# Kernel tuning notes

Hardware: AMD Instinct MI355X
Metric: run time of the kernel (lower is better)

## Reference

```python
import jax, jax.numpy as jnp
import numpy as np

OBS, ACT, HID, P, B = 128, 32, 256, 64, 4096
EPS = 1e-5


def _block(x, W, b, g, be, act=True):
    # x: [B, P, Din]; W: [P, Din, Dout]; b/g/be: [P, Dout]
    y = jnp.einsum('bpi,pio->bpo', x, W) + b
    # GroupNorm with one group per sub-policy: normalize over Dout per (b, p)
    mu = jnp.mean(y, axis=-1, keepdims=True)
    var = jnp.var(y, axis=-1, keepdims=True)
    y = (y - mu) * jax.lax.rsqrt(var + EPS) * g + be
    return jax.nn.elu(y) if act else y


def setup_inputs() -> dict:
    key = jax.random.key(0)
    ks = jax.random.split(key, 17)
    s = 0.05
    return {
        'observation': jax.random.normal(ks[0], (B, OBS), dtype=jnp.float32),
        'W1': jax.random.normal(ks[1], (P, OBS, HID), dtype=jnp.float32) * s,
        'b1': jax.random.normal(ks[2], (P, HID), dtype=jnp.float32) * s,
        'g1': jnp.ones((P, HID), dtype=jnp.float32),
        'be1': jnp.zeros((P, HID), dtype=jnp.float32),
        'W2': jax.random.normal(ks[3], (P, HID, HID), dtype=jnp.float32) * s,
        'b2': jax.random.normal(ks[4], (P, HID), dtype=jnp.float32) * s,
        'g2': jnp.ones((P, HID), dtype=jnp.float32),
        'be2': jnp.zeros((P, HID), dtype=jnp.float32),
        'W3': jax.random.normal(ks[5], (P, HID, HID), dtype=jnp.float32) * s,
        'b3': jax.random.normal(ks[6], (P, HID), dtype=jnp.float32) * s,
        'g3': jnp.ones((P, HID), dtype=jnp.float32),
        'be3': jnp.zeros((P, HID), dtype=jnp.float32),
        'W4': jax.random.normal(ks[7], (P, HID, ACT), dtype=jnp.float32) * s,
        'b4': jax.random.normal(ks[8], (P, ACT), dtype=jnp.float32) * s,
        'g4': jnp.ones((P, ACT), dtype=jnp.float32),
        'be4': jnp.zeros((P, ACT), dtype=jnp.float32),
    }


def reference(observation, W1, b1, g1, be1, W2, b2, g2, be2,
              W3, b3, g3, be3, W4, b4, g4, be4):
    # broadcast observation to each sub-policy: [B, P, OBS]
    x = jnp.broadcast_to(observation[:, None, :], (observation.shape[0], P, OBS))
    x = _block(x, W1, b1, g1, be1, act=True)
    x = _block(x, W2, b2, g2, be2, act=True)
    x = _block(x, W3, b3, g3, be3, act=True)
    x = _block(x, W4, b4, g4, be4, act=False)
    return x  # [B, P, ACT] action logits
```

## Files before the change

### kernel.cpp

```cpp
#include <hip/hip_runtime.h>

#define B_    4096
#define P_    64
#define OBS_  128
#define HID_  256
#define ACTD_ 32

typedef __attribute__((ext_vector_type(8)))  __bf16 bf16x8;
typedef __attribute__((ext_vector_type(2)))  __bf16 bf16x2_t;
typedef __attribute__((ext_vector_type(2)))  float  f32x2;
typedef __attribute__((ext_vector_type(4)))  float  f32x4;
typedef __attribute__((ext_vector_type(16))) float  f32x16;

#define XSTRIDE 264

#define WS1 0L
#define WS2 2097152L
#define WS3 6291456L
#define WS4 10485760L

#if defined(__has_builtin)
#if __has_builtin(__builtin_amdgcn_cvt_pk_bf16_f32)
#define HAVE_CVT_PK_BF16 1
#endif
#endif
#ifndef HAVE_CVT_PK_BF16
#define HAVE_CVT_PK_BF16 0
#endif

__device__ __forceinline__ unsigned short f2bf(float x) {
    unsigned u = __builtin_bit_cast(unsigned, x);
    u = (u + 0x7fffu + ((u >> 16) & 1u)) >> 16;
    return (unsigned short)u;
}

__device__ __forceinline__ unsigned pack_bf16_rne(float a, float b) {
#if HAVE_CVT_PK_BF16
    bf16x2_t p = __builtin_amdgcn_cvt_pk_bf16_f32(a, b);
    return __builtin_bit_cast(unsigned, p);
#else
    unsigned ua = __builtin_bit_cast(unsigned, a);
    unsigned ub = __builtin_bit_cast(unsigned, b);
    ua = ua + 0x7fffu + ((ua >> 16) & 1u);
    ub = ub + 0x7fffu + ((ub >> 16) & 1u);
    return __builtin_amdgcn_perm(ub, ua, 0x07060302u);
#endif
}

__device__ __forceinline__ void elu2_asm(float &a, float &b) {
    float ra, rb;
    asm volatile(
        "v_mul_f32 %0, 0x3fb8aa3b, %2\n\t"
        "v_mul_f32 %1, 0x3fb8aa3b, %3\n\t"
        "v_exp_f32 %0, %0\n\t"
        "v_exp_f32 %1, %1\n\t"
        "s_nop 0\n\t"
        "v_add_f32 %0, -1.0, %0\n\t"
        "v_add_f32 %1, -1.0, %1\n\t"
        "v_cmp_lt_f32 vcc, 0, %2\n\t"
        "v_cndmask_b32 %0, %0, %2, vcc\n\t"
        "v_cmp_lt_f32 vcc, 0, %3\n\t"
        "v_cndmask_b32 %1, %1, %3, vcc"
        : "=&v"(ra), "=&v"(rb) : "v"(a), "v"(b) : "vcc");
    a = ra; b = rb;
}

template<int K, int N>
__device__ __forceinline__ void prep_body(const float* __restrict__ W,
                                          unsigned short* __restrict__ out,
                                          int b, int t)
{
    constexpr int CH = K / 32;
    int tid  = b * 256 + t;
    int n    = tid % N;
    int rest = tid / N;
    int u    = rest % 4;
    rest    /= 4;
    int c    = rest % CH;
    int p    = rest / CH;
    const float* __restrict__ src = W + ((long)(p * K + c * 32 + u * 8)) * N + n;
    unsigned short tmp[8];
#pragma unroll
    for (int j = 0; j < 8; ++j)
        tmp[j] = f2bf(src[(long)j * N]);
    unsigned short* dst = out + ((((long)(p * CH + c) * 4 + u) * N + n) * 8);
    *reinterpret_cast<uint4*>(dst) = *reinterpret_cast<const uint4*>(tmp);
}

extern "C" __global__ __launch_bounds__(256)
void prep_all(const float* __restrict__ W1, const float* __restrict__ W2,
              const float* __restrict__ W3, const float* __restrict__ W4,
              unsigned short* __restrict__ ws)
{
    int b = blockIdx.x, t = threadIdx.x;
    if      (b < 1024) prep_body<128, 256>(W1, ws + WS1, b,        t);
    else if (b < 3072) prep_body<256, 256>(W2, ws + WS2, b - 1024, t);
    else if (b < 5120) prep_body<256, 256>(W3, ws + WS3, b - 3072, t);
    else               prep_body<256, 32 >(W4, ws + WS4, b - 5120, t);
}

template<int KCH>
__device__ __forceinline__ void layer256(
    unsigned short* __restrict__ X,
    const char* __restrict__ wsrc,
    const float* __restrict__ bp, const float* __restrict__ gp, const float* __restrict__ bep,
    float2* __restrict__ part, float2* __restrict__ stats,
    int tid, bool elu)
{
    const int w  = tid >> 6;
    const int l5 = tid & 31;
    const int h  = (tid & 63) >> 5;

    const bf16x8* __restrict__ Wp = (const bf16x8*)wsrc + (h * 256 + w * 64 + l5);
    const int nb = w * 64 + 4 * h;

    f32x16 acc[2][2];
#pragma unroll
    for (int nt = 0; nt < 2; ++nt)
#pragma unroll
        for (int q = 0; q < 4; ++q) {
            const float4 b4 = *reinterpret_cast<const float4*>(bp + nb + nt * 32 + 8 * q);
#pragma unroll
            for (int mt = 0; mt < 2; ++mt) {
                acc[nt][mt][4 * q + 0] = b4.x;
                acc[nt][mt][4 * q + 1] = b4.y;
                acc[nt][mt][4 * q + 2] = b4.z;
                acc[nt][mt][4 * q + 3] = b4.w;
            }
        }

#pragma unroll
    for (int c = 0; c < KCH; ++c) {
        const int k0 = c * 16 + h * 8;
        bf16x8 x0 = *(const bf16x8*)(X + l5 * XSTRIDE + k0);
        bf16x8 x1 = *(const bf16x8*)(X + (32 + l5) * XSTRIDE + k0);
        bf16x8 w0 = Wp[c * 512];
        bf16x8 w1 = Wp[c * 512 + 32];
        acc[0][0] = __builtin_amdgcn_mfma_f32_32x32x16_bf16(w0, x0, acc[0][0], 0, 0, 0);
        acc[0][1] = __builtin_amdgcn_mfma_f32_32x32x16_bf16(w0, x1, acc[0][1], 0, 0, 0);
        acc[1][0] = __builtin_amdgcn_mfma_f32_32x32x16_bf16(w1, x0, acc[1][0], 0, 0, 0);
        acc[1][1] = __builtin_amdgcn_mfma_f32_32x32x16_bf16(w1, x1, acc[1][1], 0, 0, 0);
    }
    __syncthreads();

    {
        f32x2 S0 = {0.f, 0.f}, S20 = {0.f, 0.f};
        f32x2 S1 = {0.f, 0.f}, S21 = {0.f, 0.f};
#pragma unroll
        for (int nt = 0; nt < 2; ++nt)
#pragma unroll
            for (int rp = 0; rp < 8; ++rp) {
                f32x2 v0 = {acc[nt][0][2 * rp], acc[nt][0][2 * rp + 1]};
                f32x2 v1 = {acc[nt][1][2 * rp], acc[nt][1][2 * rp + 1]};
                S0 += v0;  S20 = v0 * v0 + S20;
                S1 += v1;  S21 = v1 * v1 + S21;
            }
        part[l5 * 9 + w * 2 + h]        = make_float2(S0.x + S0.y, S20.x + S20.y);
        part[(32 + l5) * 9 + w * 2 + h] = make_float2(S1.x + S1.y, S21.x + S21.y);
    }
    __syncthreads();
    if (w == 0) {
        const int lane = tid & 63;
        float s = 0.f, s2 = 0.f;
#pragma unroll
        for (int i = 0; i < 8; ++i) {
            float2 pp = part[lane * 9 + i];
            s += pp.x; s2 += pp.y;
        }
        float mu  = s * (1.f / 256.f);
        float var = s2 * (1.f / 256.f) - mu * mu;
        stats[lane] = make_float2(mu, rsqrtf(var + 1e-5f));
    }
    __syncthreads();

    const float2 st0 = stats[l5], st1 = stats[32 + l5];
    const f32x2 mu0v = {st0.x, st0.x}, rs0v = {st0.y, st0.y};
    const f32x2 mu1v = {st1.x, st1.x}, rs1v = {st1.y, st1.y};
#pragma unroll
    for (int nt = 0; nt < 2; ++nt) {
#pragma unroll
        for (int q = 0; q < 4; ++q) {
            const int nq = nb + nt * 32 + 8 * q;
            const float4 g4 = *reinterpret_cast<const float4*>(gp  + nq);
            const float4 e4 = *reinterpret_cast<const float4*>(bep + nq);
            const f32x2 g01 = {g4.x, g4.y}, g23 = {g4.z, g4.w};
            const f32x2 e01 = {e4.x, e4.y}, e23 = {e4.z, e4.w};
#pragma unroll
            for (int mt = 0; mt < 2; ++mt) {
                const f32x2 mu = mt ? mu1v : mu0v;
                const f32x2 rs = mt ? rs1v : rs0v;
                f32x2 y01 = {acc[nt][mt][4 * q + 0], acc[nt][mt][4 * q + 1]};
                f32x2 y23 = {acc[nt][mt][4 * q + 2], acc[nt][mt][4 * q + 3]};
                f32x2 z01 = (y01 - mu) * rs * g01 + e01;
                f32x2 z23 = (y23 - mu) * rs * g23 + e23;
                float v0 = z01.x, v1 = z01.y, v2 = z23.x, v3 = z23.y;
                if (elu) { elu2_asm(v0, v1); elu2_asm(v2, v3); }
                uint2 pk;
                pk.x = pack_bf16_rne(v0, v1);
                pk.y = pack_bf16_rne(v2, v3);
                *reinterpret_cast<uint2*>(X + (mt * 32 + l5) * XSTRIDE + nq) = pk;
            }
        }
    }
    __syncthreads();
}

__device__ __forceinline__ void layer32(
    const unsigned short* __restrict__ X,
    const char* __restrict__ wsrc,
    const float* __restrict__ bp, const float* __restrict__ gp, const float* __restrict__ bep,
    float* __restrict__ outg, int bbase, int p, int tid)
{
    const int w = tid >> 6, lane = tid & 63, ln = lane & 15, quad = lane >> 4;
    const bf16x8* __restrict__ Bp = (const bf16x8*)wsrc + (quad * 32 + ln);

    const float bb0 = bp[ln], bb1 = bp[16 + ln];
    f32x4 acc[2];
#pragma unroll
    for (int r = 0; r < 4; ++r) { acc[0][r] = bb0; acc[1][r] = bb1; }

#pragma unroll
    for (int c = 0; c < 8; ++c) {
        bf16x8 a  = *(const bf16x8*)(X + (16 * w + ln) * XSTRIDE + c * 32 + quad * 8);
        bf16x8 b0 = Bp[c * 128];
        bf16x8 b1 = Bp[c * 128 + 16];
        acc[0] = __builtin_amdgcn_mfma_f32_16x16x32_bf16(a, b0, acc[0], 0, 0, 0);
        acc[1] = __builtin_amdgcn_mfma_f32_16x16x32_bf16(a, b1, acc[1], 0, 0, 0);
    }

    const float g0 = gp[ln], g1 = gp[16 + ln], be0 = bep[ln], be1 = bep[16 + ln];
#pragma unroll
    for (int r = 0; r < 4; ++r) {
        float y0 = acc[0][r], y1 = acc[1][r];
        float s = y0 + y1, s2 = y0 * y0 + y1 * y1;
        s += __shfl_xor(s, 1);  s2 += __shfl_xor(s2, 1);
        s += __shfl_xor(s, 2);  s2 += __shfl_xor(s2, 2);
        s += __shfl_xor(s, 4);  s2 += __shfl_xor(s2, 4);
        s += __shfl_xor(s, 8);  s2 += __shfl_xor(s2, 8);
        float mu  = s * (1.f / 32.f);
        float var = s2 * (1.f / 32.f) - mu * mu;
        float rs  = rsqrtf(var + 1e-5f);
        const int row = bbase + 16 * w + quad * 4 + r;
        float* o = outg + ((long)row * P_ + p) * ACTD_;
        o[ln]      = (y0 - mu) * rs * g0 + be0;
        o[16 + ln] = (y1 - mu) * rs * g1 + be1;
    }
}

extern "C" __global__ void __launch_bounds__(256, 4)
policy_fused(const float* __restrict__ obs,
             const unsigned short* __restrict__ wbf,
             const float* __restrict__ b1, const float* __restrict__ g1, const float* __restrict__ be1,
             const float* __restrict__ b2, const float* __restrict__ g2, const float* __restrict__ be2,
             const float* __restrict__ b3, const float* __restrict__ g3, const float* __restrict__ be3,
             const float* __restrict__ b4, const float* __restrict__ g4, const float* __restrict__ be4,
             float* __restrict__ out)
{
    __shared__ __align__(16) unsigned short X[64 * XSTRIDE];
    __shared__ float2 part[64 * 9];
    __shared__ float2 stats[64];

    const int tid = threadIdx.x;
    const int bx  = blockIdx.x;
    const int p     = ((bx & 7) << 3) | ((bx >> 3) & 7);
    const int bbase = (bx >> 6) * 64;

    const char* ws1 = (const char*)(wbf + WS1 + (long)p * (128 * 256));
    const char* ws2 = (const char*)(wbf + WS2 + (long)p * (256 * 256));
    const char* ws3 = (const char*)(wbf + WS3 + (long)p * (256 * 256));
    const char* ws4 = (const char*)(wbf + WS4 + (long)p * (256 * 32));

    for (int idx = tid; idx < 64 * 32; idx += 256) {
        int row = idx >> 5, c4 = idx & 31;
        float4 v = *reinterpret_cast<const float4*>(obs + (long)(bbase + row) * OBS_ + c4 * 4);
        uint2 pk;
        pk.x = pack_bf16_rne(v.x, v.y);
        pk.y = pack_bf16_rne(v.z, v.w);
        *reinterpret_cast<uint2*>(X + row * XSTRIDE + c4 * 4) = pk;
    }
    __syncthreads();

    layer256<8>(X, ws1, b1 + p * 256, g1 + p * 256, be1 + p * 256, part, stats, tid, true);
    layer256<16>(X, ws2, b2 + p * 256, g2 + p * 256, be2 + p * 256, part, stats, tid, true);
    layer256<16>(X, ws3, b3 + p * 256, g3 + p * 256, be3 + p * 256, part, stats, tid, true);
    layer32(X, ws4, b4 + p * 32, g4 + p * 32, be4 + p * 32, out, bbase, p, tid);
}

extern "C" void kernel_launch(void* const* d_in, const int* in_sizes, int n_in,
                              void* d_out, int out_size, void* d_ws, size_t ws_size,
                              hipStream_t stream)
{
    const float* obs = (const float*)d_in[0];
    const float* W1  = (const float*)d_in[1];
    const float* b1  = (const float*)d_in[2];
    const float* g1  = (const float*)d_in[3];
    const float* be1 = (const float*)d_in[4];
    const float* W2  = (const float*)d_in[5];
    const float* b2  = (const float*)d_in[6];
    const float* g2  = (const float*)d_in[7];
    const float* be2 = (const float*)d_in[8];
    const float* W3  = (const float*)d_in[9];
    const float* b3  = (const float*)d_in[10];
    const float* g3  = (const float*)d_in[11];
    const float* be3 = (const float*)d_in[12];
    const float* W4  = (const float*)d_in[13];
    const float* b4  = (const float*)d_in[14];
    const float* g4  = (const float*)d_in[15];
    const float* be4 = (const float*)d_in[16];
    float* out = (float*)d_out;
    unsigned short* ws = (unsigned short*)d_ws;

    hipLaunchKernelGGL(prep_all, dim3(5376), dim3(256), 0, stream, W1, W2, W3, W4, ws);

    hipLaunchKernelGGL(policy_fused, dim3(4096), dim3(256), 0, stream,
                       obs, ws,
                       b1, g1, be1, b2, g2, be2, b3, g3, be3, b4, g4, be4, out);
}
```

Before: 263.5 us.

## Double workgroup to 512 threads, halving per-wave MFMA tiles in hidden layers

Raises the fused kernel's workgroup from 4 to 8 waves. In each 256-wide layer every wave now computes one 32-column N tile instead of two, which halves accumulator registers per thread. The GroupNorm statistics reduction changes to a two-step LDS combine followed by a shuffle reduction across all threads. The final 32-wide layer leaves half the waves idle. The aim is more waves in flight to hide latency, at the cost of extra barriers and duplicated X loads from LDS across waves.

```diff
diff --git a/kernel.cpp b/kernel.cpp
--- a/kernel.cpp
+++ b/kernel.cpp
@@ -111,23 +111,21 @@
     const int l5 = tid & 31;
     const int h  = (tid & 63) >> 5;
 
-    const bf16x8* __restrict__ Wp = (const bf16x8*)wsrc + (h * 256 + w * 64 + l5);
-    const int nb = w * 64 + 4 * h;
-
-    f32x16 acc[2][2];
-#pragma unroll
-    for (int nt = 0; nt < 2; ++nt)
-#pragma unroll
-        for (int q = 0; q < 4; ++q) {
-            const float4 b4 = *reinterpret_cast<const float4*>(bp + nb + nt * 32 + 8 * q);
-#pragma unroll
-            for (int mt = 0; mt < 2; ++mt) {
-                acc[nt][mt][4 * q + 0] = b4.x;
-                acc[nt][mt][4 * q + 1] = b4.y;
-                acc[nt][mt][4 * q + 2] = b4.z;
-                acc[nt][mt][4 * q + 3] = b4.w;
-            }
+    const bf16x8* __restrict__ Wp = (const bf16x8*)wsrc + (h * 256 + w * 32 + l5);
+    const int nb = w * 32 + 4 * h;
+
+    f32x16 acc[2];
+#pragma unroll
+    for (int q = 0; q < 4; ++q) {
+        const float4 b4 = *reinterpret_cast<const float4*>(bp + nb + 8 * q);
+#pragma unroll
+        for (int mt = 0; mt < 2; ++mt) {
+            acc[mt][4 * q + 0] = b4.x;
+            acc[mt][4 * q + 1] = b4.y;
+            acc[mt][4 * q + 2] = b4.z;
+            acc[mt][4 * q + 3] = b4.w;
         }
+    }
 
 #pragma unroll
     for (int c = 0; c < KCH; ++c) {
@@ -135,41 +133,49 @@
         bf16x8 x0 = *(const bf16x8*)(X + l5 * XSTRIDE + k0);
         bf16x8 x1 = *(const bf16x8*)(X + (32 + l5) * XSTRIDE + k0);
         bf16x8 w0 = Wp[c * 512];
-        bf16x8 w1 = Wp[c * 512 + 32];
-        acc[0][0] = __builtin_amdgcn_mfma_f32_32x32x16_bf16(w0, x0, acc[0][0], 0, 0, 0);
-        acc[0][1] = __builtin_amdgcn_mfma_f32_32x32x16_bf16(w0, x1, acc[0][1], 0, 0, 0);
-        acc[1][0] = __builtin_amdgcn_mfma_f32_32x32x16_bf16(w1, x0, acc[1][0], 0, 0, 0);
-        acc[1][1] = __builtin_amdgcn_mfma_f32_32x32x16_bf16(w1, x1, acc[1][1], 0, 0, 0);
-    }
-    __syncthreads();
-
+        acc[0] = __builtin_amdgcn_mfma_f32_32x32x16_bf16(w0, x0, acc[0], 0, 0, 0);
+        acc[1] = __builtin_amdgcn_mfma_f32_32x32x16_bf16(w0, x1, acc[1], 0, 0, 0);
+    }
+
+    float2 p0, p1;
     {
         f32x2 S0 = {0.f, 0.f}, S20 = {0.f, 0.f};
         f32x2 S1 = {0.f, 0.f}, S21 = {0.f, 0.f};
 #pragma unroll
-        for (int nt = 0; nt < 2; ++nt)
-#pragma unroll
-            for (int rp = 0; rp < 8; ++rp) {
-                f32x2 v0 = {acc[nt][0][2 * rp], acc[nt][0][2 * rp + 1]};
-                f32x2 v1 = {acc[nt][1][2 * rp], acc[nt][1][2 * rp + 1]};
-                S0 += v0;  S20 = v0 * v0 + S20;
-                S1 += v1;  S21 = v1 * v1 + S21;
-            }
-        part[l5 * 9 + w * 2 + h]        = make_float2(S0.x + S0.y, S20.x + S20.y);
-        part[(32 + l5) * 9 + w * 2 + h] = make_float2(S1.x + S1.y, S21.x + S21.y);
-    }
-    __syncthreads();
-    if (w == 0) {
-        const int lane = tid & 63;
-        float s = 0.f, s2 = 0.f;
-#pragma unroll
-        for (int i = 0; i < 8; ++i) {
-            float2 pp = part[lane * 9 + i];
-            s += pp.x; s2 += pp.y;
+        for (int rp = 0; rp < 8; ++rp) {
+            f32x2 v0 = {acc[0][2 * rp], acc[0][2 * rp + 1]};
+            f32x2 v1 = {acc[1][2 * rp], acc[1][2 * rp + 1]};
+            S0 += v0;  S20 = v0 * v0 + S20;
+            S1 += v1;  S21 = v1 * v1 + S21;
         }
-        float mu  = s * (1.f / 256.f);
-        float var = s2 * (1.f / 256.f) - mu * mu;
-        stats[lane] = make_float2(mu, rsqrtf(var + 1e-5f));
+        p0 = make_float2(S0.x + S0.y, S20.x + S20.y);
+        p1 = make_float2(S1.x + S1.y, S21.x + S21.y);
+    }
+
+    if (h == 0) {
+        part[l5 * 9 + w]        = p0;
+        part[(32 + l5) * 9 + w] = p1;
+    }
+    __syncthreads();
+    if (h == 1) {
+        float2 a = part[l5 * 9 + w];
+        part[l5 * 9 + w] = make_float2(a.x + p0.x, a.y + p0.y);
+        float2 b = part[(32 + l5) * 9 + w];
+        part[(32 + l5) * 9 + w] = make_float2(b.x + p1.x, b.y + p1.y);
+    }
+    __syncthreads();
+    {
+        const int row = tid >> 3, i = tid & 7;
+        float2 pp = part[row * 9 + i];
+        float s = pp.x, s2 = pp.y;
+        s += __shfl_xor(s, 1);  s2 += __shfl_xor(s2, 1);
+        s += __shfl_xor(s, 2);  s2 += __shfl_xor(s2, 2);
+        s += __shfl_xor(s, 4);  s2 += __shfl_xor(s2, 4);
+        if (i == 0) {
+            float mu  = s * (1.f / 256.f);
+            float var = s2 * (1.f / 256.f) - mu * mu;
+            stats[row] = make_float2(mu, rsqrtf(var + 1e-5f));
+        }
     }
     __syncthreads();
 
@@ -177,29 +183,26 @@
     const f32x2 mu0v = {st0.x, st0.x}, rs0v = {st0.y, st0.y};
     const f32x2 mu1v = {st1.x, st1.x}, rs1v = {st1.y, st1.y};
 #pragma unroll
-    for (int nt = 0; nt < 2; ++nt) {
-#pragma unroll
-        for (int q = 0; q < 4; ++q) {
-            const int nq = nb + nt * 32 + 8 * q;
-            const float4 g4 = *reinterpret_cast<const float4*>(gp  + nq);
-            const float4 e4 = *reinterpret_cast<const float4*>(bep + nq);
-            const f32x2 g01 = {g4.x, g4.y}, g23 = {g4.z, g4.w};
-            const f32x2 e01 = {e4.x, e4.y}, e23 = {e4.z, e4.w};
-#pragma unroll
-            for (int mt = 0; mt < 2; ++mt) {
-                const f32x2 mu = mt ? mu1v : mu0v;
-                const f32x2 rs = mt ? rs1v : rs0v;
-                f32x2 y01 = {acc[nt][mt][4 * q + 0], acc[nt][mt][4 * q + 1]};
-                f32x2 y23 = {acc[nt][mt][4 * q + 2], acc[nt][mt][4 * q + 3]};
-                f32x2 z01 = (y01 - mu) * rs * g01 + e01;
-                f32x2 z23 = (y23 - mu) * rs * g23 + e23;
-                float v0 = z01.x, v1 = z01.y, v2 = z23.x, v3 = z23.y;
-                if (elu) { elu2_asm(v0, v1); elu2_asm(v2, v3); }
-                uint2 pk;
-                pk.x = pack_bf16_rne(v0, v1);
-                pk.y = pack_bf16_rne(v2, v3);
-                *reinterpret_cast<uint2*>(X + (mt * 32 + l5) * XSTRIDE + nq) = pk;
-            }
+    for (int q = 0; q < 4; ++q) {
+        const int nq = nb + 8 * q;
+        const float4 g4 = *reinterpret_cast<const float4*>(gp  + nq);
+        const float4 e4 = *reinterpret_cast<const float4*>(bep + nq);
+        const f32x2 g01 = {g4.x, g4.y}, g23 = {g4.z, g4.w};
+        const f32x2 e01 = {e4.x, e4.y}, e23 = {e4.z, e4.w};
+#pragma unroll
+        for (int mt = 0; mt < 2; ++mt) {
+            const f32x2 mu = mt ? mu1v : mu0v;
+            const f32x2 rs = mt ? rs1v : rs0v;
+            f32x2 y01 = {acc[mt][4 * q + 0], acc[mt][4 * q + 1]};
+            f32x2 y23 = {acc[mt][4 * q + 2], acc[mt][4 * q + 3]};
+            f32x2 z01 = (y01 - mu) * rs * g01 + e01;
+            f32x2 z23 = (y23 - mu) * rs * g23 + e23;
+            float v0 = z01.x, v1 = z01.y, v2 = z23.x, v3 = z23.y;
+            if (elu) { elu2_asm(v0, v1); elu2_asm(v2, v3); }
+            uint2 pk;
+            pk.x = pack_bf16_rne(v0, v1);
+            pk.y = pack_bf16_rne(v2, v3);
+            *reinterpret_cast<uint2*>(X + (mt * 32 + l5) * XSTRIDE + nq) = pk;
         }
     }
     __syncthreads();
@@ -211,7 +214,9 @@
     const float* __restrict__ bp, const float* __restrict__ gp, const float* __restrict__ bep,
     float* __restrict__ outg, int bbase, int p, int tid)
 {
-    const int w = tid >> 6, lane = tid & 63, ln = lane & 15, quad = lane >> 4;
+    const int w = tid >> 6;
+    if (w >= 4) return;
+    const int lane = tid & 63, ln = lane & 15, quad = lane >> 4;
     const bf16x8* __restrict__ Bp = (const bf16x8*)wsrc + (quad * 32 + ln);
 
     const float bb0 = bp[ln], bb1 = bp[16 + ln];
@@ -247,7 +252,7 @@
     }
 }
 
-extern "C" __global__ void __launch_bounds__(256, 4)
+extern "C" __global__ void __launch_bounds__(512, 8)
 policy_fused(const float* __restrict__ obs,
              const unsigned short* __restrict__ wbf,
              const float* __restrict__ b1, const float* __restrict__ g1, const float* __restrict__ be1,
@@ -270,7 +275,7 @@
     const char* ws3 = (const char*)(wbf + WS3 + (long)p * (256 * 256));
     const char* ws4 = (const char*)(wbf + WS4 + (long)p * (256 * 32));
 
-    for (int idx = tid; idx < 64 * 32; idx += 256) {
+    for (int idx = tid; idx < 64 * 32; idx += 512) {
         int row = idx >> 5, c4 = idx & 31;
         float4 v = *reinterpret_cast<const float4*>(obs + (long)(bbase + row) * OBS_ + c4 * 4);
         uint2 pk;
@@ -312,7 +317,7 @@
 
     hipLaunchKernelGGL(prep_all, dim3(5376), dim3(256), 0, stream, W1, W2, W3, W4, ws);
 
-    hipLaunchKernelGGL(policy_fused, dim3(4096), dim3(256), 0, stream,
+    hipLaunchKernelGGL(policy_fused, dim3(4096), dim3(512), 0, stream,
                        obs, ws,
                        b1, g1, be1, b2, g2, be2, b3, g3, be3, b4, g4, be4, out);
 }
```

Result: slower. 270.4 us (+2.6%).
